# Performance work log

Hardware: AMD Instinct MI355X
Metric: run time of the kernel (lower is better)

Reference implementation:

```python
import jax, jax.numpy as jnp
import numpy as np

IN_F, OUT_F = 768, 2304
E, R = 8, 16            # num adapters, lora rank
ALPHA = 32
SCALING = ALPHA / R
GATE_DIM = 64


def setup_inputs() -> dict:
    key = jax.random.key(0)
    ks = jax.random.split(key, 8)
    B, S = 8, 2048
    x = jax.random.normal(ks[0], (B, S, IN_F), dtype=jnp.float32)
    z = jax.random.normal(ks[1], (B, GATE_DIM), dtype=jnp.float32)
    # frozen linear (nn.Linear weight layout [out, in])
    W = jax.random.normal(ks[2], (OUT_F, IN_F), dtype=jnp.float32) * 0.02
    b = jax.random.normal(ks[3], (OUT_F,), dtype=jnp.float32) * 0.02
    # stacked LoRA adapters: A [E, r, in], B [E, out, r]
    A = jax.random.normal(ks[4], (E, R, IN_F), dtype=jnp.float32) * (1.0 / np.sqrt(IN_F))
    Bm = jax.random.normal(ks[5], (E, OUT_F, R), dtype=jnp.float32) * 0.02
    # spectral gate: linear + softmax over experts
    Wg = jax.random.normal(ks[6], (E, GATE_DIM), dtype=jnp.float32) * 0.1
    bg = jax.random.normal(ks[7], (E,), dtype=jnp.float32) * 0.1
    return {"x": x, "z": z, "W": W, "b": b, "A": A, "Bm": Bm, "Wg": Wg, "bg": bg}


def reference(x, z, W, b, A, Bm, Wg, bg):
    # frozen linear: [B,S,out]
    frozen_out = jnp.einsum('bsi,oi->bso', x, W) + b
    # gate weights over adapters: [B,E]
    gate_w = jax.nn.softmax(jnp.einsum('bg,eg->be', z, Wg) + bg, axis=-1)
    # fused adapters: down-proj to rank r per expert (dropout p=0 -> identity)
    h = jnp.einsum('bsi,eri->bser', x, A)               # [B,S,E,r] small (r=16)
    # up-proj + gate-weighted sum over experts, fused into one contraction
    adapt = jnp.einsum('bser,eor,be->bso', h, Bm, gate_w) * SCALING
    return frozen_out + adapt
```

## Files before the change

### kernel.cpp

```cpp
#include <hip/hip_runtime.h>
#include <hip/hip_bf16.h>
#include <stdint.h>

typedef unsigned short u16;
typedef __attribute__((ext_vector_type(8))) short short8;
typedef __attribute__((ext_vector_type(4))) float floatx4;

#define M_TOT 16384
#define N_OUT 2304
#define KX    768
#define KL    128
#define SCALING 2.0f

#define XBLKS   6144
#define WBLKS   864
#define ABLKS   48
#define BMRBLKS 144
#define PREP_BLOCKS (XBLKS + WBLKS + ABLKS + BMRBLKS + 1)

__device__ __forceinline__ u16 f2b(float f) {
  union { __hip_bfloat16 h; u16 u; } c; c.h = __float2bfloat16(f); return c.u;
}
__device__ __forceinline__ float ldf(const void* p, long i, bool f32) {
  if (f32) return ((const float*)p)[i];
  union { u16 u; __hip_bfloat16 h; } c; c.u = ((const u16*)p)[i];
  return __bfloat162float(c.h);
}

__device__ __forceinline__ void gload_lds16(const void* g, void* l) {
  __builtin_amdgcn_global_load_lds(
      (const __attribute__((address_space(1))) void*)g,
      (__attribute__((address_space(3))) void*)l, 16, 0, 0);
}

__device__ __forceinline__ void cvt8(const void* src, u16* dst, long i, bool f32) {
  u16 v[8];
  if (f32) {
    const float4* s = (const float4*)src;
    float4 a = s[i * 2], b = s[i * 2 + 1];
    v[0] = f2b(a.x); v[1] = f2b(a.y); v[2] = f2b(a.z); v[3] = f2b(a.w);
    v[4] = f2b(b.x); v[5] = f2b(b.y); v[6] = f2b(b.z); v[7] = f2b(b.w);
  } else {
    *(uint4*)v = ((const uint4*)src)[i];
  }
  ((uint4*)dst)[i] = *(uint4*)v;
}

__global__ __launch_bounds__(256) void prep_kernel(
    const void* __restrict__ x,  const void* __restrict__ W,
    const void* __restrict__ A,  const void* __restrict__ Bm,
    const void* __restrict__ z,  const void* __restrict__ Wg,
    const void* __restrict__ bg,
    u16* __restrict__ xbf, u16* __restrict__ Wbf, u16* __restrict__ Abf,
    u16* __restrict__ bmr, float* __restrict__ gsc, int* __restrict__ flagp) {
  __shared__ int s_flag;
  const int tid = threadIdx.x;
  if (tid < 64) {
    u16 v = ((const u16*)x)[tid * 2];
    int e = (v >> 7) & 0xFF;
    int huge = (e >= 160) ? 1 : 0;
    for (int off = 1; off < 64; off <<= 1) huge += __shfl_xor(huge, off, 64);
    if (tid == 0) s_flag = (huge >= 4) ? 1 : 0;
  }
  __syncthreads();
  const bool f32 = (s_flag != 0);

  int b = blockIdx.x;
  if (b < XBLKS) {
    cvt8(x, xbf, (long)b * 256 + tid, f32);
  } else if (b < XBLKS + WBLKS) {
    cvt8(W, Wbf, (long)(b - XBLKS) * 256 + tid, f32);
  } else if (b < XBLKS + WBLKS + ABLKS) {
    cvt8(A, Abf, (long)(b - XBLKS - WBLKS) * 256 + tid, f32);
  } else if (b < XBLKS + WBLKS + ABLKS + BMRBLKS) {
    long i0 = ((long)(b - XBLKS - WBLKS - ABLKS) * 256 + tid) * 8;
    u16 v[8];
#pragma unroll
    for (int j = 0; j < 8; ++j) {
      long idx = i0 + j;
      long o = idx >> 7, er = idx & 127;
      long e = er >> 4, r = er & 15;
      v[j] = f2b(ldf(Bm, (e * 2304 + o) * 16 + r, f32));
    }
    *(uint4*)&bmr[i0] = *(uint4*)v;
  } else {
    if (tid == 0) *flagp = s_flag;
    if (tid < 64) {
      const int bb = tid >> 3, e = tid & 7;
      float acc = ldf(bg, e, f32);
      for (int i = 0; i < 64; ++i)
        acc += ldf(z, bb * 64 + i, f32) * ldf(Wg, e * 64 + i, f32);
      float mx = acc;
      for (int off = 1; off < 8; off <<= 1) mx = fmaxf(mx, __shfl_xor(mx, off, 64));
      float ex = __expf(acc - mx);
      float sm = ex;
      for (int off = 1; off < 8; off <<= 1) sm += __shfl_xor(sm, off, 64);
      gsc[tid] = (ex / sm) * SCALING;
    }
  }
}

__global__ __launch_bounds__(256) void gemm_h(
    const u16* __restrict__ xbf, const u16* __restrict__ Abf,
    const float* __restrict__ gsc, u16* __restrict__ hg) {
  __shared__ __align__(128) u16 As[128][64];
  __shared__ __align__(128) u16 Bs[128][64];
  const int tid = threadIdx.x, wave = tid >> 6, lane = tid & 63;
  const int wm = wave >> 1, wn = wave & 1;
  const int quad = lane >> 4, l16 = lane & 15;
  const int srow = lane >> 3, scol = (lane & 7) * 8;
  const int m0 = blockIdx.x * 128;

  floatx4 acc[4][4];
#pragma unroll
  for (int i = 0; i < 4; ++i)
#pragma unroll
    for (int j = 0; j < 4; ++j) acc[i][j] = floatx4{0.f, 0.f, 0.f, 0.f};

  for (int kb = 0; kb < 12; ++kb) {
    const int kc = kb * 64;
#pragma unroll
    for (int j = 0; j < 4; ++j) {
      int r = wave * 32 + j * 8 + srow;
      gload_lds16(xbf + (size_t)(m0 + r) * KX + kc + scol,
                  (char*)(&As[0][0]) + (wave * 32 + j * 8) * 128);
      gload_lds16(Abf + (size_t)r * KX + kc + scol,
                  (char*)(&Bs[0][0]) + (wave * 32 + j * 8) * 128);
    }
    __syncthreads();
#pragma unroll
    for (int ks = 0; ks < 2; ++ks) {
      short8 af[4], bf[4];
#pragma unroll
      for (int mi = 0; mi < 4; ++mi)
        af[mi] = *(const short8*)&As[wm * 64 + mi * 16 + l16][ks * 32 + quad * 8];
#pragma unroll
      for (int ni = 0; ni < 4; ++ni)
        bf[ni] = *(const short8*)&Bs[wn * 64 + ni * 16 + l16][ks * 32 + quad * 8];
#pragma unroll
      for (int mi = 0; mi < 4; ++mi)
#pragma unroll
        for (int ni = 0; ni < 4; ++ni)
          acc[mi][ni] = __builtin_amdgcn_mfma_f32_16x16x32_bf16(af[mi], bf[ni], acc[mi][ni], 0, 0, 0);
    }
    __syncthreads();
  }
  const int bb = m0 >> 11;
  float gv[4];
#pragma unroll
  for (int ni = 0; ni < 4; ++ni) gv[ni] = gsc[bb * 8 + wn * 4 + ni];
#pragma unroll
  for (int mi = 0; mi < 4; ++mi) {
    int rbase = m0 + wm * 64 + mi * 16 + quad * 4;
#pragma unroll
    for (int ni = 0; ni < 4; ++ni) {
      int c = wn * 64 + ni * 16 + l16;
#pragma unroll
      for (int t = 0; t < 4; ++t)
        hg[(size_t)(rbase + t) * KL + c] = f2b(acc[mi][ni][t] * gv[ni]);
    }
  }
}

__global__ __launch_bounds__(256) void gemm_main(
    const u16* __restrict__ xbf, const u16* __restrict__ hg,
    const u16* __restrict__ Wbf, const u16* __restrict__ bmr,
    const void* __restrict__ bias, void* __restrict__ outv,
    const int* __restrict__ flagp) {
  __shared__ __align__(128) u16 As[128][64];
  __shared__ __align__(128) u16 Bs[128][64];
  const int tid = threadIdx.x, wave = tid >> 6, lane = tid & 63;
  const int wm = wave >> 1, wn = wave & 1;
  const int quad = lane >> 4, l16 = lane & 15;
  const int srow = lane >> 3, scol = (lane & 7) * 8;

  const int linear = blockIdx.x;
  const int xcd = linear & 7;
  const int g = linear >> 3;
  const int m_idx = xcd * 16 + (g & 15);
  const int n_idx = g >> 4;
  const int m0 = m_idx * 128;
  const int n0 = n_idx * 128;

  floatx4 acc[4][4];
#pragma unroll
  for (int i = 0; i < 4; ++i)
#pragma unroll
    for (int j = 0; j < 4; ++j) acc[i][j] = floatx4{0.f, 0.f, 0.f, 0.f};

  for (int kb = 0; kb < 14; ++kb) {
    const u16* ap; const u16* bp; int lda, ldb, kc;
    if (kb < 12) { ap = xbf; lda = KX; bp = Wbf; ldb = KX; kc = kb * 64; }
    else         { ap = hg;  lda = KL; bp = bmr; ldb = KL; kc = (kb - 12) * 64; }
#pragma unroll
    for (int j = 0; j < 4; ++j) {
      int r = wave * 32 + j * 8 + srow;
      gload_lds16(ap + (size_t)(m0 + r) * lda + kc + scol,
                  (char*)(&As[0][0]) + (wave * 32 + j * 8) * 128);
      gload_lds16(bp + (size_t)(n0 + r) * ldb + kc + scol,
                  (char*)(&Bs[0][0]) + (wave * 32 + j * 8) * 128);
    }
    __syncthreads();
#pragma unroll
    for (int ks = 0; ks < 2; ++ks) {
      short8 af[4], bf[4];
#pragma unroll
      for (int mi = 0; mi < 4; ++mi)
        af[mi] = *(const short8*)&As[wm * 64 + mi * 16 + l16][ks * 32 + quad * 8];
#pragma unroll
      for (int ni = 0; ni < 4; ++ni)
        bf[ni] = *(const short8*)&Bs[wn * 64 + ni * 16 + l16][ks * 32 + quad * 8];
#pragma unroll
      for (int mi = 0; mi < 4; ++mi)
#pragma unroll
        for (int ni = 0; ni < 4; ++ni)
          acc[mi][ni] = __builtin_amdgcn_mfma_f32_16x16x32_bf16(af[mi], bf[ni], acc[mi][ni], 0, 0, 0);
    }
    __syncthreads();
  }

  const bool f32 = (*flagp != 0);
  float bv[4];
#pragma unroll
  for (int ni = 0; ni < 4; ++ni)
    bv[ni] = ldf(bias, n0 + wn * 64 + ni * 16 + l16, f32);
#pragma unroll
  for (int mi = 0; mi < 4; ++mi) {
    int rbase = m0 + wm * 64 + mi * 16 + quad * 4;
#pragma unroll
    for (int ni = 0; ni < 4; ++ni) {
      int c = n0 + wn * 64 + ni * 16 + l16;
#pragma unroll
      for (int t = 0; t < 4; ++t) {
        float v = acc[mi][ni][t] + bv[ni];
        size_t idx = (size_t)(rbase + t) * N_OUT + c;
        if (f32) __builtin_nontemporal_store(v, (float*)outv + idx);
        else     __builtin_nontemporal_store(f2b(v), (u16*)outv + idx);
      }
    }
  }
}

extern "C" void kernel_launch(void* const* d_in, const int* in_sizes, int n_in,
                              void* d_out, int out_size, void* d_ws, size_t ws_size,
                              hipStream_t stream) {
  const void* x  = d_in[0];
  const void* z  = d_in[1];
  const void* W  = d_in[2];
  const void* bb = d_in[3];
  const void* A  = d_in[4];
  const void* Bm = d_in[5];
  const void* Wg = d_in[6];
  const void* bg = d_in[7];

  char* ws = (char*)d_ws;
  int*   flag = (int*)ws;
  float* gsc  = (float*)(ws + 256);
  u16*   xbf  = (u16*)(ws + 1024);
  u16*   Wbf  = (u16*)(ws + 1024 + 25165824ull);
  u16*   Abf  = (u16*)(ws + 1024 + 25165824ull + 3538944ull);
  u16*   bmr  = (u16*)(ws + 1024 + 25165824ull + 3538944ull + 196608ull);
  u16*   hg   = (u16*)(ws + 1024 + 25165824ull + 3538944ull + 196608ull + 589824ull);

  prep_kernel<<<PREP_BLOCKS, 256, 0, stream>>>(
      x, W, A, Bm, z, Wg, bg, xbf, Wbf, Abf, bmr, gsc, flag);

  gemm_h<<<M_TOT / 128, 256, 0, stream>>>(xbf, Abf, gsc, hg);

  gemm_main<<<(N_OUT / 128) * (M_TOT / 128), 256, 0, stream>>>(
      xbf, hg, Wbf, bmr, bb, d_out, flag);
}
```

Before: 134.3 us.

## Rewrite main GEMM as 256x256 double-buffered pipelined tile with swizzled LDS

The main GEMM goes from 128x128 tiles with a single LDS buffer and 64-wide K steps to 256x256 tiles using 8 waves, 128-wide K steps and double-buffered LDS. Global-to-LDS loads for the next tiles are issued in halves and interleaved with MFMA phases under barriers, with s_setprio raising MFMA priority. LDS columns are XOR-swizzled to avoid bank conflicts. This aims to hide load latency and raise arithmetic intensity, at the cost of much higher register and LDS pressure, fewer blocks in the grid, and a fragile waitcnt schedule.

```diff
diff --git a/kernel.cpp b/kernel.cpp
--- a/kernel.cpp
+++ b/kernel.cpp
@@ -11,6 +11,7 @@
 #define KX    768
 #define KL    128
 #define SCALING 2.0f
+#define NTILES 14
 
 #define XBLKS   6144
 #define WBLKS   864
@@ -162,61 +163,148 @@
   }
 }
 
-__global__ __launch_bounds__(256) void gemm_main(
+
+#define KX2 1536
+#define KL2 256
+
+__device__ __forceinline__ void stage_half(const u16* src, int ldab, int row0,
+                                           int kcb, char* ldsTile, int half,
+                                           int wave, int lane) {
+#pragma unroll
+  for (int j = 0; j < 2; ++j) {
+    const int chunk = half * 16384 + (wave * 2 + j) * 1024;
+    const int q = chunk + lane * 16;
+    const int row = q >> 7;
+    const int col = (q & 127) ^ ((row & 7) << 4);
+    gload_lds16((const char*)src + (size_t)(row0 + row) * ldab + kcb + col,
+                ldsTile + chunk);
+  }
+}
+
+__device__ __forceinline__ short8 ldfrag(const char* tile, int row, int colb) {
+  return *(const short8*)(tile + row * 128 + (colb ^ ((row & 7) << 4)));
+}
+
+#define MFMA16(a, b, c) __builtin_amdgcn_mfma_f32_16x16x32_bf16(a, b, c, 0, 0, 0)
+#define BAR() __builtin_amdgcn_s_barrier()
+#define LGKM0() asm volatile("s_waitcnt lgkmcnt(0)" ::: "memory")
+
+template <int BUF>
+__device__ __forceinline__ void tile_step(
+    int t, const u16* xbf, const u16* hg, const u16* Wbf, const u16* bmr,
+    int m0, int n0, int wave, int lane, int wm, int wn, int quad, int l16,
+    char* As0, char* Bs0, floatx4 (&acc)[8][4]) {
+  char* At = As0 + BUF * 32768;
+  char* Bt = Bs0 + BUF * 32768;
+  char* Ao = As0 + (BUF ^ 1) * 32768;
+  char* Bo = Bs0 + (BUF ^ 1) * 32768;
+  const bool stg1 = (t + 1 < NTILES), stg2 = (t + 2 < NTILES);
+  const u16 *a1p = xbf, *b1p = Wbf, *a2p = xbf, *b2p = Wbf;
+  int lda1 = KX2, ldb1 = KX2, kc1 = (t + 1) * 128;
+  int lda2 = KX2, ldb2 = KX2, kc2 = (t + 2) * 128;
+  if (t + 1 >= 12) { a1p = hg; b1p = bmr; lda1 = KL2; ldb1 = KL2; kc1 = (t + 1 - 12) * 128; }
+  if (t + 2 >= 12) { a2p = hg; b2p = bmr; lda2 = KL2; ldb2 = KL2; kc2 = (t + 2 - 12) * 128; }
+  const int arow = wm * 128, brow = wn * 64;
+
+  short8 a[8], b0[4], b1[4];
+
+#pragma unroll
+  for (int mi = 0; mi < 8; ++mi) a[mi] = ldfrag(At, arow + mi * 16 + l16, quad * 16);
+  b0[0] = ldfrag(Bt, brow + l16, quad * 16);
+  b0[1] = ldfrag(Bt, brow + 16 + l16, quad * 16);
+  if (stg1) stage_half(a1p, lda1, m0, kc1, Ao, 1, wave, lane);
+  BAR(); LGKM0();
+  __builtin_amdgcn_s_setprio(1);
+#pragma unroll
+  for (int mi = 0; mi < 8; ++mi) {
+    acc[mi][0] = MFMA16(a[mi], b0[0], acc[mi][0]);
+    acc[mi][1] = MFMA16(a[mi], b0[1], acc[mi][1]);
+  }
+  __builtin_amdgcn_s_setprio(0);
+  BAR();
+
+  b0[2] = ldfrag(Bt, brow + 32 + l16, quad * 16);
+  b0[3] = ldfrag(Bt, brow + 48 + l16, quad * 16);
+#pragma unroll
+  for (int ni = 0; ni < 4; ++ni)
+    b1[ni] = ldfrag(Bt, brow + ni * 16 + l16, 64 + quad * 16);
+  if (stg1) stage_half(b1p, ldb1, n0, kc1, Bo, 1, wave, lane);
+  BAR(); LGKM0();
+  __builtin_amdgcn_s_setprio(1);
+#pragma unroll
+  for (int mi = 0; mi < 8; ++mi) {
+    acc[mi][2] = MFMA16(a[mi], b0[2], acc[mi][2]);
+    acc[mi][3] = MFMA16(a[mi], b0[3], acc[mi][3]);
+  }
+  __builtin_amdgcn_s_setprio(0);
+  BAR();
+
+#pragma unroll
+  for (int mi = 0; mi < 8; ++mi) a[mi] = ldfrag(At, arow + mi * 16 + l16, 64 + quad * 16);
+  if (stg2) stage_half(b2p, ldb2, n0, kc2, Bt, 0, wave, lane);
+  BAR(); LGKM0();
+  __builtin_amdgcn_s_setprio(1);
+#pragma unroll
+  for (int mi = 0; mi < 8; ++mi) {
+    acc[mi][0] = MFMA16(a[mi], b1[0], acc[mi][0]);
+    acc[mi][1] = MFMA16(a[mi], b1[1], acc[mi][1]);
+  }
+  __builtin_amdgcn_s_setprio(0);
+  BAR();
+
+  if (stg2) stage_half(a2p, lda2, m0, kc2, At, 0, wave, lane);
+  BAR();
+  __builtin_amdgcn_s_setprio(1);
+#pragma unroll
+  for (int mi = 0; mi < 8; ++mi) {
+    acc[mi][2] = MFMA16(a[mi], b1[2], acc[mi][2]);
+    acc[mi][3] = MFMA16(a[mi], b1[3], acc[mi][3]);
+  }
+  __builtin_amdgcn_s_setprio(0);
+  if (stg2) asm volatile("s_waitcnt vmcnt(4)" ::: "memory");
+  else      asm volatile("s_waitcnt vmcnt(0)" ::: "memory");
+  BAR();
+}
+
+__global__ __launch_bounds__(512, 2) void gemm_main(
     const u16* __restrict__ xbf, const u16* __restrict__ hg,
     const u16* __restrict__ Wbf, const u16* __restrict__ bmr,
     const void* __restrict__ bias, void* __restrict__ outv,
     const int* __restrict__ flagp) {
-  __shared__ __align__(128) u16 As[128][64];
-  __shared__ __align__(128) u16 Bs[128][64];
+  __shared__ __align__(1024) u16 As[2][16384];
+  __shared__ __align__(1024) u16 Bs[2][16384];
+
   const int tid = threadIdx.x, wave = tid >> 6, lane = tid & 63;
-  const int wm = wave >> 1, wn = wave & 1;
+  const int wm = wave >> 2, wn = wave & 3;
   const int quad = lane >> 4, l16 = lane & 15;
-  const int srow = lane >> 3, scol = (lane & 7) * 8;
-
-  const int linear = blockIdx.x;
-  const int xcd = linear & 7;
-  const int g = linear >> 3;
-  const int m_idx = xcd * 16 + (g & 15);
-  const int n_idx = g >> 4;
-  const int m0 = m_idx * 128;
-  const int n0 = n_idx * 128;
-
-  floatx4 acc[4][4];
-#pragma unroll
-  for (int i = 0; i < 4; ++i)
+
+  const int bid = blockIdx.x;
+  const int xcd = bid & 7, g = bid >> 3;
+  const int m0 = (xcd * 8 + (g & 7)) * 256;
+  const int n0 = (g >> 3) * 256;
+
+  char* As0 = (char*)&As[0][0];
+  char* Bs0 = (char*)&Bs[0][0];
+
+  floatx4 acc[8][4];
+#pragma unroll
+  for (int i = 0; i < 8; ++i)
 #pragma unroll
     for (int j = 0; j < 4; ++j) acc[i][j] = floatx4{0.f, 0.f, 0.f, 0.f};
 
-  for (int kb = 0; kb < 14; ++kb) {
-    const u16* ap; const u16* bp; int lda, ldb, kc;
-    if (kb < 12) { ap = xbf; lda = KX; bp = Wbf; ldb = KX; kc = kb * 64; }
-    else         { ap = hg;  lda = KL; bp = bmr; ldb = KL; kc = (kb - 12) * 64; }
-#pragma unroll
-    for (int j = 0; j < 4; ++j) {
-      int r = wave * 32 + j * 8 + srow;
-      gload_lds16(ap + (size_t)(m0 + r) * lda + kc + scol,
-                  (char*)(&As[0][0]) + (wave * 32 + j * 8) * 128);
-      gload_lds16(bp + (size_t)(n0 + r) * ldb + kc + scol,
-                  (char*)(&Bs[0][0]) + (wave * 32 + j * 8) * 128);
-    }
-    __syncthreads();
-#pragma unroll
-    for (int ks = 0; ks < 2; ++ks) {
-      short8 af[4], bf[4];
-#pragma unroll
-      for (int mi = 0; mi < 4; ++mi)
-        af[mi] = *(const short8*)&As[wm * 64 + mi * 16 + l16][ks * 32 + quad * 8];
-#pragma unroll
-      for (int ni = 0; ni < 4; ++ni)
-        bf[ni] = *(const short8*)&Bs[wn * 64 + ni * 16 + l16][ks * 32 + quad * 8];
-#pragma unroll
-      for (int mi = 0; mi < 4; ++mi)
-#pragma unroll
-        for (int ni = 0; ni < 4; ++ni)
-          acc[mi][ni] = __builtin_amdgcn_mfma_f32_16x16x32_bf16(af[mi], bf[ni], acc[mi][ni], 0, 0, 0);
-    }
-    __syncthreads();
+  stage_half(xbf, KX2, m0, 0, As0, 0, wave, lane);
+  stage_half(Wbf, KX2, n0, 0, Bs0, 0, wave, lane);
+  stage_half(xbf, KX2, m0, 0, As0, 1, wave, lane);
+  stage_half(Wbf, KX2, n0, 0, Bs0, 1, wave, lane);
+  stage_half(Wbf, KX2, n0, 128, Bs0 + 32768, 0, wave, lane);
+  stage_half(xbf, KX2, m0, 128, As0 + 32768, 0, wave, lane);
+  asm volatile("s_waitcnt vmcnt(4)" ::: "memory");
+  BAR();
+
+#pragma unroll 1
+  for (int tt = 0; tt < 7; ++tt) {
+    tile_step<0>(tt * 2,     xbf, hg, Wbf, bmr, m0, n0, wave, lane, wm, wn, quad, l16, As0, Bs0, acc);
+    tile_step<1>(tt * 2 + 1, xbf, hg, Wbf, bmr, m0, n0, wave, lane, wm, wn, quad, l16, As0, Bs0, acc);
   }
 
   const bool f32 = (*flagp != 0);
@@ -225,15 +313,15 @@
   for (int ni = 0; ni < 4; ++ni)
     bv[ni] = ldf(bias, n0 + wn * 64 + ni * 16 + l16, f32);
 #pragma unroll
-  for (int mi = 0; mi < 4; ++mi) {
-    int rbase = m0 + wm * 64 + mi * 16 + quad * 4;
+  for (int mi = 0; mi < 8; ++mi) {
+    int rbase = m0 + wm * 128 + mi * 16 + quad * 4;
 #pragma unroll
     for (int ni = 0; ni < 4; ++ni) {
       int c = n0 + wn * 64 + ni * 16 + l16;
 #pragma unroll
-      for (int t = 0; t < 4; ++t) {
-        float v = acc[mi][ni][t] + bv[ni];
-        size_t idx = (size_t)(rbase + t) * N_OUT + c;
+      for (int u = 0; u < 4; ++u) {
+        float v = acc[mi][ni][u] + bv[ni];
+        size_t idx = (size_t)(rbase + u) * N_OUT + c;
         if (f32) __builtin_nontemporal_store(v, (float*)outv + idx);
         else     __builtin_nontemporal_store(f2b(v), (u16*)outv + idx);
       }
@@ -267,6 +355,6 @@
 
   gemm_h<<<M_TOT / 128, 256, 0, stream>>>(xbf, Abf, gsc, hg);
 
-  gemm_main<<<(N_OUT / 128) * (M_TOT / 128), 256, 0, stream>>>(
+  gemm_main<<<(N_OUT / 256) * (M_TOT / 256), 512, 0, stream>>>(
       xbf, hg, Wbf, bmr, bb, d_out, flag);
 }
```

After: 158.1 us. 1.18x slower.

## Fold gated LoRA adapters into per-batch combined weight matrices

Applied to the files above, without the earlier changes.

Replaces the separate low-rank path (an x·A GEMM producing gated h, then two extra K-steps in the main GEMM) with a precomputed per-batch combined weight W + Σ_e g_e·B_e·A_e. A new small GEMM kernel builds these eight combined matrices from the transposed A and the gate-scaled B. The main GEMM then runs only the 12 K-steps over x. This drops the full pass over x in the h kernel and the rank-128 tail of the main loop. In exchange it writes and reads eight 2304x768 bf16 weight copies, and rounding the combined weight to bf16 changes precision slightly.

```diff
diff --git a/kernel.cpp b/kernel.cpp
--- a/kernel.cpp
+++ b/kernel.cpp
@@ -21,10 +21,13 @@
 __device__ __forceinline__ u16 f2b(float f) {
   union { __hip_bfloat16 h; u16 u; } c; c.h = __float2bfloat16(f); return c.u;
 }
+__device__ __forceinline__ float b2f(u16 u) {
+  union { u16 u; __hip_bfloat16 h; } c; c.u = u;
+  return __bfloat162float(c.h);
+}
 __device__ __forceinline__ float ldf(const void* p, long i, bool f32) {
   if (f32) return ((const float*)p)[i];
-  union { u16 u; __hip_bfloat16 h; } c; c.u = ((const u16*)p)[i];
-  return __bfloat162float(c.h);
+  return b2f(((const u16*)p)[i]);
 }
 
 __device__ __forceinline__ void gload_lds16(const void* g, void* l) {
@@ -51,7 +54,7 @@
     const void* __restrict__ A,  const void* __restrict__ Bm,
     const void* __restrict__ z,  const void* __restrict__ Wg,
     const void* __restrict__ bg,
-    u16* __restrict__ xbf, u16* __restrict__ Wbf, u16* __restrict__ Abf,
+    u16* __restrict__ xbf, u16* __restrict__ Wbf, u16* __restrict__ Atr,
     u16* __restrict__ bmr, float* __restrict__ gsc, int* __restrict__ flagp) {
   __shared__ int s_flag;
   const int tid = threadIdx.x;
@@ -71,7 +74,13 @@
   } else if (b < XBLKS + WBLKS) {
     cvt8(W, Wbf, (long)(b - XBLKS) * 256 + tid, f32);
   } else if (b < XBLKS + WBLKS + ABLKS) {
-    cvt8(A, Abf, (long)(b - XBLKS - WBLKS) * 256 + tid, f32);
+    long c0 = (long)(b - XBLKS - WBLKS) * 256 + tid;
+    long er = c0 / 96, i0 = (c0 % 96) * 8;
+    u16 v[8];
+#pragma unroll
+    for (int j = 0; j < 8; ++j) v[j] = f2b(ldf(A, er * 768 + i0 + j, f32));
+#pragma unroll
+    for (int j = 0; j < 8; ++j) Atr[(i0 + j) * 128 + er] = v[j];
   } else if (b < XBLKS + WBLKS + ABLKS + BMRBLKS) {
     long i0 = ((long)(b - XBLKS - WBLKS - ABLKS) * 256 + tid) * 8;
     u16 v[8];
@@ -100,16 +109,25 @@
   }
 }
 
-__global__ __launch_bounds__(256) void gemm_h(
-    const u16* __restrict__ xbf, const u16* __restrict__ Abf,
-    const float* __restrict__ gsc, u16* __restrict__ hg) {
+__global__ __launch_bounds__(256) void wcomb_kernel(
+    const u16* __restrict__ bmr, const u16* __restrict__ Atr,
+    const u16* __restrict__ Wbf, const float* __restrict__ gsc,
+    u16* __restrict__ wc) {
   __shared__ __align__(128) u16 As[128][64];
   __shared__ __align__(128) u16 Bs[128][64];
+  __shared__ float sg[8];
   const int tid = threadIdx.x, wave = tid >> 6, lane = tid & 63;
   const int wm = wave >> 1, wn = wave & 1;
   const int quad = lane >> 4, l16 = lane & 15;
   const int srow = lane >> 3, scol = (lane & 7) * 8;
-  const int m0 = blockIdx.x * 128;
+
+  int bid = blockIdx.x;
+  const int nt = bid % 6; bid /= 6;
+  const int mt = bid % 18; const int b = bid / 18;
+  const int m0 = mt * 128, n0 = nt * 128;
+
+  if (tid < 8) sg[tid] = gsc[b * 8 + tid];
+  __syncthreads();
 
   floatx4 acc[4][4];
 #pragma unroll
@@ -117,15 +135,24 @@
 #pragma unroll
     for (int j = 0; j < 4; ++j) acc[i][j] = floatx4{0.f, 0.f, 0.f, 0.f};
 
-  for (int kb = 0; kb < 12; ++kb) {
+  for (int kb = 0; kb < 2; ++kb) {
     const int kc = kb * 64;
 #pragma unroll
     for (int j = 0; j < 4; ++j) {
       int r = wave * 32 + j * 8 + srow;
-      gload_lds16(xbf + (size_t)(m0 + r) * KX + kc + scol,
+      gload_lds16(bmr + (size_t)(m0 + r) * 128 + kc + scol,
                   (char*)(&As[0][0]) + (wave * 32 + j * 8) * 128);
-      gload_lds16(Abf + (size_t)r * KX + kc + scol,
-                  (char*)(&Bs[0][0]) + (wave * 32 + j * 8) * 128);
+    }
+#pragma unroll
+    for (int j = 0; j < 4; ++j) {
+      int c = j * 256 + tid;
+      int row = c >> 3, ch = c & 7;
+      u16 v[8];
+      *(uint4*)v = *(const uint4*)&Atr[(size_t)(n0 + row) * 128 + kc + ch * 8];
+      float g = sg[(kc + ch * 8) >> 4];
+#pragma unroll
+      for (int t = 0; t < 8; ++t) v[t] = f2b(b2f(v[t]) * g);
+      *(uint4*)&Bs[row][ch * 8] = *(uint4*)v;
     }
     __syncthreads();
 #pragma unroll
@@ -145,26 +172,24 @@
     }
     __syncthreads();
   }
-  const int bb = m0 >> 11;
-  float gv[4];
-#pragma unroll
-  for (int ni = 0; ni < 4; ++ni) gv[ni] = gsc[bb * 8 + wn * 4 + ni];
+  u16* wcb = wc + (size_t)b * N_OUT * KX;
 #pragma unroll
   for (int mi = 0; mi < 4; ++mi) {
     int rbase = m0 + wm * 64 + mi * 16 + quad * 4;
 #pragma unroll
     for (int ni = 0; ni < 4; ++ni) {
-      int c = wn * 64 + ni * 16 + l16;
-#pragma unroll
-      for (int t = 0; t < 4; ++t)
-        hg[(size_t)(rbase + t) * KL + c] = f2b(acc[mi][ni][t] * gv[ni]);
+      int c = n0 + wn * 64 + ni * 16 + l16;
+#pragma unroll
+      for (int t = 0; t < 4; ++t) {
+        float v = acc[mi][ni][t] + b2f(Wbf[(size_t)(rbase + t) * KX + c]);
+        wcb[(size_t)(rbase + t) * KX + c] = f2b(v);
+      }
     }
   }
 }
 
 __global__ __launch_bounds__(256) void gemm_main(
-    const u16* __restrict__ xbf, const u16* __restrict__ hg,
-    const u16* __restrict__ Wbf, const u16* __restrict__ bmr,
+    const u16* __restrict__ xbf, const u16* __restrict__ wc,
     const void* __restrict__ bias, void* __restrict__ outv,
     const int* __restrict__ flagp) {
   __shared__ __align__(128) u16 As[128][64];
@@ -181,6 +206,7 @@
   const int n_idx = g >> 4;
   const int m0 = m_idx * 128;
   const int n0 = n_idx * 128;
+  const u16* wcb = wc + (size_t)(m0 >> 11) * N_OUT * KX;
 
   floatx4 acc[4][4];
 #pragma unroll
@@ -188,16 +214,14 @@
 #pragma unroll
     for (int j = 0; j < 4; ++j) acc[i][j] = floatx4{0.f, 0.f, 0.f, 0.f};
 
-  for (int kb = 0; kb < 14; ++kb) {
-    const u16* ap; const u16* bp; int lda, ldb, kc;
-    if (kb < 12) { ap = xbf; lda = KX; bp = Wbf; ldb = KX; kc = kb * 64; }
-    else         { ap = hg;  lda = KL; bp = bmr; ldb = KL; kc = (kb - 12) * 64; }
+  for (int kb = 0; kb < 12; ++kb) {
+    const int kc = kb * 64;
 #pragma unroll
     for (int j = 0; j < 4; ++j) {
       int r = wave * 32 + j * 8 + srow;
-      gload_lds16(ap + (size_t)(m0 + r) * lda + kc + scol,
+      gload_lds16(xbf + (size_t)(m0 + r) * KX + kc + scol,
                   (char*)(&As[0][0]) + (wave * 32 + j * 8) * 128);
-      gload_lds16(bp + (size_t)(n0 + r) * ldb + kc + scol,
+      gload_lds16(wcb + (size_t)(n0 + r) * KX + kc + scol,
                   (char*)(&Bs[0][0]) + (wave * 32 + j * 8) * 128);
     }
     __syncthreads();
@@ -258,15 +282,15 @@
   float* gsc  = (float*)(ws + 256);
   u16*   xbf  = (u16*)(ws + 1024);
   u16*   Wbf  = (u16*)(ws + 1024 + 25165824ull);
-  u16*   Abf  = (u16*)(ws + 1024 + 25165824ull + 3538944ull);
+  u16*   Atr  = (u16*)(ws + 1024 + 25165824ull + 3538944ull);
   u16*   bmr  = (u16*)(ws + 1024 + 25165824ull + 3538944ull + 196608ull);
-  u16*   hg   = (u16*)(ws + 1024 + 25165824ull + 3538944ull + 196608ull + 589824ull);
+  u16*   wcp  = (u16*)(ws + 1024 + 25165824ull + 3538944ull + 196608ull + 589824ull);
 
   prep_kernel<<<PREP_BLOCKS, 256, 0, stream>>>(
-      x, W, A, Bm, z, Wg, bg, xbf, Wbf, Abf, bmr, gsc, flag);
-
-  gemm_h<<<M_TOT / 128, 256, 0, stream>>>(xbf, Abf, gsc, hg);
+      x, W, A, Bm, z, Wg, bg, xbf, Wbf, Atr, bmr, gsc, flag);
+
+  wcomb_kernel<<<8 * 18 * 6, 256, 0, stream>>>(bmr, Atr, Wbf, gsc, wcp);
 
   gemm_main<<<(N_OUT / 128) * (M_TOT / 128), 256, 0, stream>>>(
-      xbf, hg, Wbf, bmr, bb, d_out, flag);
-}
+      xbf, wcp, bb, d_out, flag);
+}
```

After: 152.6 us. +13.6%, slower.
